# Performance work log

Measured on AMD Instinct MI355X. Metric: run time of the kernel, lower is better.

The kernel has to match this reference:

```python
import jax, jax.numpy as jnp
import numpy as np

B, L, H, E = 16, 4096, 3, 512   # q: [B, L, H, E]; in_channels = H*E = 1536
M = 128                          # number of selected frequency modes
F_LEN = L // 2 + 1               # rfft length


def setup_inputs() -> dict:
    key = jax.random.key(0)
    kq, kr, ki = jax.random.split(key, 3)
    q = jax.random.normal(kq, (B, L, H, E), dtype=jnp.float32)
    # get_frequency_modes('random'): shuffle range(L//2), take M, sort (distinct modes)
    rng = np.random.default_rng(0)
    index = jnp.asarray(np.sort(rng.permutation(L // 2)[:M]).astype(np.int32))
    # torch.rand on cfloat samples real & imag uniform[0,1); scale = 1/(in*out)
    scale = 1.0 / float((H * E) * (H * E))
    w_real = scale * jax.random.uniform(kr, (H, E, E, M), dtype=jnp.float32)
    w_imag = scale * jax.random.uniform(ki, (H, E, E, M), dtype=jnp.float32)
    return {"q": q, "w_real": w_real, "w_imag": w_imag, "index": index, "mask": 0}


def reference(q, w_real, w_imag, index, mask):
    # mask is unused by FourierBlock.forward (matches original)
    w = (w_real + 1j * w_imag).astype(jnp.complex64)      # [H, E_in, E_out, M]
    x = jnp.transpose(q, (0, 2, 3, 1))                    # [B, H, E, L]
    x_ft = jnp.fft.rfft(x, axis=-1)                       # [B, H, E, F_LEN] complex64
    # gather selected modes, batched complex matmul over all modes at once
    x_sel = x_ft[..., index]                              # [B, H, E_in, M]
    out_sel = jnp.einsum('bhim,hiom->bhom', x_sel, w)     # [B, H, E_out, M]
    # scatter back into zero-initialized spectrum
    out_ft = jnp.zeros((B, H, E, F_LEN), dtype=jnp.complex64).at[..., index].set(out_sel)
    x_out = jnp.fft.irfft(out_ft, n=L, axis=-1)           # [B, H, E, L] float32
    return x_out
```

## Files before the change

### kernel.cpp

```cpp
#include <hip/hip_runtime.h>
#include <hip/hip_bf16.h>


#define L_TOT 4096

typedef __attribute__((ext_vector_type(4))) float f32x4;
typedef __attribute__((ext_vector_type(2))) float f32x2;
typedef __attribute__((ext_vector_type(2))) unsigned u32x2;
typedef __attribute__((ext_vector_type(8))) short s16x8;
typedef __attribute__((ext_vector_type(4))) unsigned short u16x4;

__device__ __forceinline__ unsigned short f2bf(float f) {
    unsigned u = __builtin_bit_cast(unsigned, f);
    u = (u + 0x7fffu + ((u >> 16) & 1u)) >> 16;
    return (unsigned short)u;
}

__device__ __forceinline__ void gload_lds16(const void* g, void* l) {
    __builtin_amdgcn_global_load_lds((const __attribute__((address_space(1))) void*)g,
                                     (__attribute__((address_space(3))) void*)l,
                                     16, 0, 0);
}

__global__ __launch_bounds__(256) void build_ta(const int* __restrict__ index,
                                                unsigned short* __restrict__ T_A) {
    const int idx = blockIdx.x * 256 + threadIdx.x;
    const int m2 = idx >> 12;
    const int l  = idx & (L_TOT - 1);
    const int k  = index[m2 >> 1];
    const int tt = (k * l) & (L_TOT - 1);
    const float x = (float)tt * (1.0f / 2048.0f);
    T_A[idx] = f2bf((m2 & 1) ? -sinpif(x) : cospif(x));
}

__global__ __launch_bounds__(256) void build_tc(const int* __restrict__ index,
                                                unsigned short* __restrict__ T_C) {
    const int idx = blockIdx.x * 256 + threadIdx.x;
    const int l  = idx >> 8;
    const int m2 = idx & 255;
    const int k  = index[m2 >> 1];
    const int tt = (k * l) & (L_TOT - 1);
    const float x = (float)tt * (1.0f / 2048.0f);
    const float s = (k == 0 ? 1.0f : 2.0f) * (1.0f / (float)L_TOT);
    T_C[idx] = f2bf(s * ((m2 & 1) ? -sinpif(x) : cospif(x)));
}

__global__ __launch_bounds__(256) void gemm_a(const float* __restrict__ q,
                                              const unsigned short* __restrict__ T_A,
                                              unsigned short* __restrict__ Xbf) {
    __shared__ unsigned short As[64 * 64];
    __shared__ unsigned short Bs[256 * 64];

    const int bid = blockIdx.x;
    const int b   = bid / 24;
    const int cht = bid % 24;
    const int ch0 = cht * 64;
    const int h   = ch0 >> 9;
    const int i0  = ch0 & 511;
    const int t   = threadIdx.x;
    const int lane = t & 63;
    const int w    = t >> 6;
    const int chq  = t & 15;
    const int lg   = t >> 4;

    const float* qb = q + (size_t)b * L_TOT * 1536 + ch0 + chq * 4;

    f32x4 acc[4][4];
#pragma unroll
    for (int mi = 0; mi < 4; ++mi)
#pragma unroll
        for (int ni = 0; ni < 4; ++ni) acc[mi][ni] = (f32x4)0.0f;

    for (int kt = 0; kt < L_TOT; kt += 64) {
        __syncthreads();
#pragma unroll
        for (int p = 0; p < 8; ++p) {
            const int u = p * 256 + t;
            const int row = u >> 3, c16 = u & 7;
            const unsigned short* src = T_A + (size_t)row * L_TOT + kt + ((c16 ^ (row & 7)) * 8);
            unsigned short* dst = Bs + (size_t)(p * 256 + w * 64) * 8;
            gload_lds16(src, dst);
        }
        f32x4 v[4];
#pragma unroll
        for (int r = 0; r < 4; ++r)
            v[r] = *reinterpret_cast<const f32x4*>(qb + (size_t)(kt + lg * 4 + r) * 1536);
#pragma unroll
        for (int j = 0; j < 4; ++j) {
            const int c = chq * 4 + j;
            uint2 pk;
            pk.x = f2bf(v[0][j]) | ((unsigned)f2bf(v[1][j]) << 16);
            pk.y = f2bf(v[2][j]) | ((unsigned)f2bf(v[3][j]) << 16);
            *reinterpret_cast<uint2*>(As + c * 64 + ((lg * 4) ^ ((c & 7) << 3))) = pk;
        }
        __syncthreads();

#pragma unroll
        for (int kk = 0; kk < 2; ++kk) {
            const int c16 = kk * 4 + (lane >> 4);
            s16x8 af[4], bfr[4];
#pragma unroll
            for (int mi = 0; mi < 4; ++mi) {
                const int row = mi * 16 + (lane & 15);
                af[mi] = *reinterpret_cast<const s16x8*>(As + row * 64 + ((c16 ^ (row & 7)) * 8));
            }
#pragma unroll
            for (int ni = 0; ni < 4; ++ni) {
                const int row = w * 64 + ni * 16 + (lane & 15);
                bfr[ni] = *reinterpret_cast<const s16x8*>(Bs + row * 64 + ((c16 ^ (row & 7)) * 8));
            }
#pragma unroll
            for (int mi = 0; mi < 4; ++mi)
#pragma unroll
                for (int ni = 0; ni < 4; ++ni)
                    acc[mi][ni] = __builtin_amdgcn_mfma_f32_16x16x32_bf16(af[mi], bfr[ni], acc[mi][ni], 0, 0, 0);
        }
    }

    const size_t cbase = (((size_t)h * 16 + b) * 512 + i0) * 256;
#pragma unroll
    for (int mi = 0; mi < 4; ++mi) {
        const int r0 = mi * 16 + (lane >> 4) * 4;
#pragma unroll
        for (int ni = 0; ni < 4; ++ni) {
            const int col = w * 64 + ni * 16 + (lane & 15);
#pragma unroll
            for (int j = 0; j < 4; ++j)
                Xbf[cbase + (size_t)(r0 + j) * 256 + col] = f2bf(acc[mi][ni][j]);
        }
    }
}

template <int MODE>
__global__ __launch_bounds__(256) void gemm_bf16(const unsigned short* __restrict__ A,
                                                 const unsigned short* __restrict__ Bt,
                                                 void* __restrict__ Cv) {
    constexpr int BM   = 128;
    constexpr int BK   = 64;
    constexpr int KTOT = 256;
    constexpr int LDAB = 256;
    constexpr int LDC  = 4096;
    constexpr int MFR  = BM / 32;
    constexpr int APASS = BM * 8 / 256;
    constexpr int BPASS = 4;

    __shared__ unsigned short As[BM * BK];
    __shared__ unsigned short Bs[128 * BK];

    const int t = threadIdx.x;
    const int lane = t & 63;
    const int w = t >> 6;
    const int wr = w >> 1, wc = w & 1;

    const int mt = blockIdx.x >> 5, nt = blockIdx.x & 31;
    const unsigned short* Ab = A + (size_t)mt * 128 * 256;
    const unsigned short* Bb = Bt + (size_t)nt * 128 * 256;
    const size_t cbase = (size_t)mt * 128 * 4096 + nt * 128;

    f32x4 acc[MFR][4];
#pragma unroll
    for (int mi = 0; mi < MFR; ++mi)
#pragma unroll
        for (int ni = 0; ni < 4; ++ni) acc[mi][ni] = (f32x4)0.0f;

    for (int kt = 0; kt < KTOT; kt += BK) {
        __syncthreads();
#pragma unroll
        for (int p = 0; p < APASS; ++p) {
            const int u = p * 256 + t;
            const int row = u >> 3, c16 = u & 7;
            const unsigned short* src = Ab + (size_t)row * LDAB + kt + ((c16 ^ (row & 7)) * 8);
            unsigned short* dst = As + (size_t)(p * 256 + w * 64) * 8;
            gload_lds16(src, dst);
        }
#pragma unroll
        for (int p = 0; p < BPASS; ++p) {
            const int u = p * 256 + t;
            const int row = u >> 3, c16 = u & 7;
            const unsigned short* src = Bb + (size_t)row * LDAB + kt + ((c16 ^ (row & 7)) * 8);
            unsigned short* dst = Bs + (size_t)(p * 256 + w * 64) * 8;
            gload_lds16(src, dst);
        }
        __syncthreads();

#pragma unroll
        for (int kk = 0; kk < 2; ++kk) {
            const int c16 = kk * 4 + (lane >> 4);
            s16x8 af[MFR], bfr[4];
#pragma unroll
            for (int mi = 0; mi < MFR; ++mi) {
                const int row = wr * (BM / 2) + mi * 16 + (lane & 15);
                af[mi] = *reinterpret_cast<const s16x8*>(As + row * BK + ((c16 ^ (row & 7)) * 8));
            }
#pragma unroll
            for (int ni = 0; ni < 4; ++ni) {
                const int row = wc * 64 + ni * 16 + (lane & 15);
                bfr[ni] = *reinterpret_cast<const s16x8*>(Bs + row * BK + ((c16 ^ (row & 7)) * 8));
            }
#pragma unroll
            for (int mi = 0; mi < MFR; ++mi)
#pragma unroll
                for (int ni = 0; ni < 4; ++ni)
                    acc[mi][ni] = __builtin_amdgcn_mfma_f32_16x16x32_bf16(af[mi], bfr[ni], acc[mi][ni], 0, 0, 0);
        }
    }

#pragma unroll
    for (int mi = 0; mi < MFR; ++mi) {
        const int r0 = wr * (BM / 2) + mi * 16 + (lane >> 4) * 4;
#pragma unroll
        for (int ni = 0; ni < 4; ++ni) {
            const int col = wc * 64 + ni * 16 + (lane & 15);
#pragma unroll
            for (int j = 0; j < 4; ++j)
                ((float*)Cv)[cbase + (size_t)(r0 + j) * LDC + col] = acc[mi][ni][j];
        }
    }
}

__global__ __launch_bounds__(256, 3) void stage_b(const unsigned short* __restrict__ Xbf,
                                                  const float* __restrict__ wr,
                                                  const float* __restrict__ wi,
                                                  unsigned short* __restrict__ Y0,
                                                  unsigned short* __restrict__ P1) {
    __shared__ float Wl[2][8][4][128];
    const int bid = blockIdx.x;
    const int ic  = bid / 384;
    const int g   = bid % 384;
    const int h   = g >> 7;
    const int ot  = g & 127;
    const int t    = threadIdx.x;
    const int lane = t & 63;
    const int w    = t >> 6;
    const int b0   = w * 4;
    const int o0   = ot * 4;
    const int i_lo = ic * 256;

    const float* wr_base = wr + (size_t)h * 33554432 + (size_t)o0 * 128;
    const float* wi_base = wi + (size_t)h * 33554432 + (size_t)o0 * 128;
    const unsigned short* x0 = Xbf + (size_t)(h * 16 + b0) * 512 * 256 + lane * 4;

    float aR[4][4][2], aI[4][4][2];
#pragma unroll
    for (int bb = 0; bb < 4; ++bb)
#pragma unroll
        for (int oo = 0; oo < 4; ++oo) {
            aR[bb][oo][0] = aR[bb][oo][1] = 0.f;
            aI[bb][oo][0] = aI[bb][oo][1] = 0.f;
        }

#pragma unroll 1
    for (int c = 0; c < 32; ++c) {
        const int ib = i_lo + c * 8;
        __syncthreads();
#pragma unroll
        for (int p = 0; p < 4; ++p) {
            const int u = p * 256 + t;
            const int row = u >> 5;
            const int col = u & 31;
            const int ii = row >> 2, oo = row & 3;
            const size_t goff = (size_t)(ib + ii) * 65536 + oo * 128 + col * 4;
            gload_lds16(wr_base + goff, (char*)&Wl[0][0][0][0] + (size_t)u * 16);
            gload_lds16(wi_base + goff, (char*)&Wl[1][0][0][0] + (size_t)u * 16);
        }
        __syncthreads();

#pragma unroll
        for (int i = 0; i < 8; ++i) {
            u32x2 xv[4];
#pragma unroll
            for (int bb = 0; bb < 4; ++bb)
                xv[bb] = *reinterpret_cast<const u32x2*>(x0 + (size_t)bb * 131072 + (size_t)(ib + i) * 256);
            f32x2 wrv[4], wiv[4];
#pragma unroll
            for (int oo = 0; oo < 4; ++oo) {
                wrv[oo] = *reinterpret_cast<const f32x2*>(&Wl[0][i][oo][lane * 2]);
                wiv[oo] = *reinterpret_cast<const f32x2*>(&Wl[1][i][oo][lane * 2]);
            }
#pragma unroll
            for (int bb = 0; bb < 4; ++bb) {
                float xr[2], xi[2];
#pragma unroll
                for (int mm = 0; mm < 2; ++mm) {
                    const unsigned xu = xv[bb][mm];
                    xr[mm] = __builtin_bit_cast(float, xu << 16);
                    xi[mm] = __builtin_bit_cast(float, xu & 0xffff0000u);
                }
#pragma unroll
                for (int oo = 0; oo < 4; ++oo)
#pragma unroll
                    for (int mm = 0; mm < 2; ++mm) {
                        const float wrj = wrv[oo][mm];
                        const float wij = wiv[oo][mm];
                        aR[bb][oo][mm] = fmaf(xr[mm], wrj, aR[bb][oo][mm]);
                        aR[bb][oo][mm] = fmaf(-xi[mm], wij, aR[bb][oo][mm]);
                        aI[bb][oo][mm] = fmaf(xr[mm], wij, aI[bb][oo][mm]);
                        aI[bb][oo][mm] = fmaf(xi[mm], wrj, aI[bb][oo][mm]);
                    }
            }
        }
    }

    unsigned short* yout = ic ? P1 : Y0;
#pragma unroll
    for (int bb = 0; bb < 4; ++bb)
#pragma unroll
        for (int oo = 0; oo < 4; ++oo) {
            const size_t row = ((size_t)(b0 + bb) * 3 + h) * 512 + o0 + oo;
            u32x2 pk;
            pk.x = f2bf(aR[bb][oo][0]) | ((unsigned)f2bf(aI[bb][oo][0]) << 16);
            pk.y = f2bf(aR[bb][oo][1]) | ((unsigned)f2bf(aI[bb][oo][1]) << 16);
            *reinterpret_cast<u32x2*>(reinterpret_cast<char*>(yout) + row * 512 + lane * 8) = pk;
        }
}

__global__ __launch_bounds__(256) void reduce_y(unsigned short* __restrict__ Ybf,
                                                const unsigned short* __restrict__ P1) {
    const int idx = blockIdx.x * 256 + threadIdx.x;
    const uint4 a = reinterpret_cast<const uint4*>(Ybf)[idx];
    const uint4 b = reinterpret_cast<const uint4*>(P1)[idx];
    const unsigned av[4] = {a.x, a.y, a.z, a.w};
    const unsigned bv[4] = {b.x, b.y, b.z, b.w};
    unsigned rv[4];
#pragma unroll
    for (int j = 0; j < 4; ++j) {
        const float xr = __builtin_bit_cast(float, av[j] << 16);
        const float xi = __builtin_bit_cast(float, av[j] & 0xffff0000u);
        const float yr = __builtin_bit_cast(float, bv[j] << 16);
        const float yi = __builtin_bit_cast(float, bv[j] & 0xffff0000u);
        rv[j] = f2bf(xr + yr) | ((unsigned)f2bf(xi + yi) << 16);
    }
    uint4 r;
    r.x = rv[0]; r.y = rv[1]; r.z = rv[2]; r.w = rv[3];
    reinterpret_cast<uint4*>(Ybf)[idx] = r;
}

extern "C" void kernel_launch(void* const* d_in, const int* in_sizes, int n_in,
                              void* d_out, int out_size, void* d_ws, size_t ws_size,
                              hipStream_t stream) {
    const float* q     = (const float*)d_in[0];
    const float* w_re  = (const float*)d_in[1];
    const float* w_im  = (const float*)d_in[2];
    const int*   index = (const int*)d_in[3];

    char* ws = (char*)d_ws;
    unsigned short* Xbf = (unsigned short*)(ws);
    unsigned short* P1  = (unsigned short*)(ws + 12582912);
    unsigned short* Ybf = (unsigned short*)(ws + 25165824);
    unsigned short* T_A = (unsigned short*)(ws + 37748736);
    unsigned short* T_C = (unsigned short*)(ws + 39845888);

    build_ta<<<4096, 256, 0, stream>>>(index, T_A);
    build_tc<<<4096, 256, 0, stream>>>(index, T_C);
    gemm_a<<<384, 256, 0, stream>>>(q, T_A, Xbf);
    stage_b<<<768, 256, 0, stream>>>(Xbf, w_re, w_im, Ybf, P1);
    reduce_y<<<3072, 256, 0, stream>>>(Ybf, P1);
    gemm_bf16<1><<<6144, 256, 0, stream>>>(Ybf, T_C, (void*)d_out);
}
```

Measured before the change: 529.7 us.

## Double-buffer weight and X tiles in LDS with async prefetch in stage_b

Restructures the stage_b mode-mixing loop into a double-buffered pipeline. Each step handles 2 input channels instead of 8, and the next step's weight tiles and the X activations are prefetched into LDS via global_load_lds while the current step computes. X was previously read straight from global memory inside the inner loop; it is now staged through LDS too. The aim is to hide global-load latency behind FMA work, at the cost of more loop iterations and barriers, a manual vmcnt wait, and extra LDS use that could affect occupancy at 3 blocks per CU.

Measured after the change: 482.2 us. 9.0% less time.

```diff
diff --git a/kernel.cpp b/kernel.cpp
--- a/kernel.cpp
+++ b/kernel.cpp
@@ -223,7 +223,8 @@
                                                   const float* __restrict__ wi,
                                                   unsigned short* __restrict__ Y0,
                                                   unsigned short* __restrict__ P1) {
-    __shared__ float Wl[2][8][4][128];
+    __shared__ float          Wl[2][2][2][4][128];
+    __shared__ unsigned short Xl[2][16][2][256];
     const int bid = blockIdx.x;
     const int ic  = bid / 384;
     const int g   = bid % 384;
@@ -238,7 +239,26 @@
 
     const float* wr_base = wr + (size_t)h * 33554432 + (size_t)o0 * 128;
     const float* wi_base = wi + (size_t)h * 33554432 + (size_t)o0 * 128;
-    const unsigned short* x0 = Xbf + (size_t)(h * 16 + b0) * 512 * 256 + lane * 4;
+    const unsigned short* x_base = Xbf + (size_t)h * 16 * 512 * 256;
+
+    const int wsi  = t >> 7;
+    const int wso  = (t >> 5) & 3;
+    const int wsc  = t & 31;
+#define SBS(BUF, IB)                                                           \
+    {                                                                          \
+        const size_t gw = (size_t)((IB) + wsi) * 65536 + wso * 128 + wsc * 4;  \
+        char* ldsW = (char*)Wl + (BUF) * 8192 + t * 16;                        \
+        gload_lds16(wr_base + gw, ldsW);                                       \
+        gload_lds16(wi_base + gw, ldsW + 4096);                                \
+        _Pragma("unroll")                                                      \
+        for (int pp = 0; pp < 4; ++pp) {                                       \
+            const int u2 = pp * 256 + t;                                       \
+            const int xb = u2 >> 6, xi = (u2 >> 5) & 1, xc = u2 & 31;          \
+            const unsigned short* gx = x_base + (size_t)xb * 131072            \
+                                       + (size_t)((IB) + xi) * 256 + xc * 8;   \
+            gload_lds16(gx, (char*)Xl + (BUF) * 16384 + (size_t)u2 * 16);      \
+        }                                                                      \
+    }
 
     float aR[4][4][2], aI[4][4][2];
 #pragma unroll
@@ -249,33 +269,33 @@
             aI[bb][oo][0] = aI[bb][oo][1] = 0.f;
         }
 
+    SBS(0, i_lo);
+
 #pragma unroll 1
-    for (int c = 0; c < 32; ++c) {
-        const int ib = i_lo + c * 8;
-        __syncthreads();
-#pragma unroll
-        for (int p = 0; p < 4; ++p) {
-            const int u = p * 256 + t;
-            const int row = u >> 5;
-            const int col = u & 31;
-            const int ii = row >> 2, oo = row & 3;
-            const size_t goff = (size_t)(ib + ii) * 65536 + oo * 128 + col * 4;
-            gload_lds16(wr_base + goff, (char*)&Wl[0][0][0][0] + (size_t)u * 16);
-            gload_lds16(wi_base + goff, (char*)&Wl[1][0][0][0] + (size_t)u * 16);
-        }
-        __syncthreads();
-
-#pragma unroll
-        for (int i = 0; i < 8; ++i) {
+    for (int c = 0; c < 128; ++c) {
+        const int ib = i_lo + c * 2;
+        const int p  = c & 1;
+        const int ibn = (c + 1 < 128) ? (ib + 2) : i_lo;
+        SBS(p ^ 1, ibn);
+        __builtin_amdgcn_sched_barrier(0);
+        asm volatile("s_waitcnt vmcnt(6)" ::: "memory");
+        __builtin_amdgcn_sched_barrier(0);
+        __builtin_amdgcn_s_barrier();
+        __builtin_amdgcn_sched_barrier(0);
+#pragma unroll
+        for (int i = 0; i < 2; ++i) {
             u32x2 xv[4];
 #pragma unroll
             for (int bb = 0; bb < 4; ++bb)
-                xv[bb] = *reinterpret_cast<const u32x2*>(x0 + (size_t)bb * 131072 + (size_t)(ib + i) * 256);
+                xv[bb] = *reinterpret_cast<const u32x2*>(
+                    (char*)Xl + p * 16384 + (b0 + bb) * 1024 + i * 512 + lane * 8);
             f32x2 wrv[4], wiv[4];
 #pragma unroll
             for (int oo = 0; oo < 4; ++oo) {
-                wrv[oo] = *reinterpret_cast<const f32x2*>(&Wl[0][i][oo][lane * 2]);
-                wiv[oo] = *reinterpret_cast<const f32x2*>(&Wl[1][i][oo][lane * 2]);
+                wrv[oo] = *reinterpret_cast<const f32x2*>(
+                    (char*)Wl + p * 8192 + i * 2048 + oo * 512 + lane * 8);
+                wiv[oo] = *reinterpret_cast<const f32x2*>(
+                    (char*)Wl + p * 8192 + 4096 + i * 2048 + oo * 512 + lane * 8);
             }
 #pragma unroll
             for (int bb = 0; bb < 4; ++bb) {
@@ -299,6 +319,8 @@
                     }
             }
         }
+        __builtin_amdgcn_sched_barrier(0);
+        __builtin_amdgcn_s_barrier();
     }
 
     unsigned short* yout = ic ? P1 : Y0;
```
